# Optimization experiments

Measured on AMD Instinct MI355X. Metric: run time of the kernel, lower is better.

Reference implementation:

```python
import jax, jax.numpy as jnp
import numpy as np

B, N, D, H, L = 8, 1025, 1024, 8, 2   # N = maxlen + 1
NUM_BUCKETS = 64
EPS = 1e-8


def layernorm(x):
    mu = jnp.mean(x, axis=-1, keepdims=True)
    var = jnp.mean((x - mu) ** 2, axis=-1, keepdims=True)
    return (x - mu) / jnp.sqrt(var + EPS)


def rmsnorm(x):
    return x * jax.lax.rsqrt(jnp.mean(x * x, axis=-1, keepdims=True) + EPS)


def rel_attn_bias(action_ts, ts_w, pos_w):
    # positional part: pos_w[j - i + N - 1]  (equivalent to the pad/repeat trick)
    idx = jnp.arange(N)[None, :] - jnp.arange(N)[:, None] + (N - 1)  # [N,N] in [0,2N-2]
    rel_pos = pos_w[idx][None]  # [1,N,N]
    # time part: bucketize ext[i+1] - ext[j], ext = cat(ts, ts[:, N-1:N])
    ext = jnp.concatenate([action_ts, action_ts[:, N - 1:N]], axis=1)  # [B,N+1]
    diff = ext[:, 1:, None] - ext[:, None, :-1]  # [B,N,N]
    bucket = (jnp.log(jnp.clip(jnp.abs(diff), 1, None).astype(jnp.float32)) / 0.301).astype(jnp.int32)
    bucket = jnp.clip(bucket, 0, NUM_BUCKETS)
    rel_ts = ts_w[bucket]  # [B,N,N]
    return rel_pos + rel_ts


def hstu_block(x, mask, bias, qkvu, out_w, out_b, fc1_w, fc1_b, fc2_w, fc2_b):
    hd = D // H
    xn = layernorm(x)
    qkvu_act = jax.nn.silu(xn @ qkvu)  # [B,N,4D]
    q, k, v, u = jnp.split(qkvu_act, 4, axis=-1)
    q = q.reshape(B, N, H, hd)
    k = k.reshape(B, N, H, hd)
    v = v.reshape(B, N, H, hd)
    scores = jnp.einsum('bihd,bjhd->bhij', q, k) + bias[:, None]  # [B,H,N,N]
    attn = jax.nn.silu(scores) / N * mask[:, None]
    av = jnp.einsum('bhij,bjhd->bihd', attn, v).reshape(B, N, D)
    attn_out = (u * layernorm(av)) @ out_w + out_b
    h = x + attn_out
    # SwiGLU FFN (mult=2) with RMSNorm pre-norm and residual
    vg = rmsnorm(h) @ fc1_w + fc1_b  # [B,N,4D]
    vv, g = jnp.split(vg, 2, axis=-1)
    y = (jax.nn.silu(g) * vv) @ fc2_w + fc2_b
    return h + y


def setup_inputs() -> dict:
    key = jax.random.key(0)
    ks = jax.random.split(key, 12)
    std = 0.02
    seqs = jax.random.normal(ks[0], (B, N, D), jnp.float32)
    mask = jnp.tril(jnp.ones((N, N), jnp.float32))[None].repeat(B, axis=0)
    action_ts = jnp.sort(jax.random.randint(ks[1], (B, N), 0, 1000000000).astype(jnp.int64), axis=1)
    return {
        'seqs': seqs,
        'mask': mask,
        'action_ts': action_ts,
        'qkvu': jax.random.normal(ks[2], (L, D, 4 * D), jnp.float32) * std,
        'out_w': jax.random.normal(ks[3], (L, D, D), jnp.float32) * std,
        'out_b': jnp.zeros((L, D), jnp.float32),
        'ts_w': jax.random.normal(ks[4], (L, NUM_BUCKETS + 1), jnp.float32) * std,
        'pos_w': jax.random.normal(ks[5], (L, 2 * N - 1), jnp.float32) * std,
        'fc1_w': jax.random.normal(ks[6], (L, D, 4 * D), jnp.float32) * std,
        'fc1_b': jnp.zeros((L, 4 * D), jnp.float32),
        'fc2_w': jax.random.normal(ks[7], (L, 2 * D, D), jnp.float32) * std,
        'fc2_b': jnp.zeros((L, D), jnp.float32),
    }


def reference(seqs, mask, action_ts, qkvu, out_w, out_b, ts_w, pos_w, fc1_w, fc1_b, fc2_w, fc2_b):
    h = seqs
    for l in range(L):
        bias = rel_attn_bias(action_ts, ts_w[l], pos_w[l])
        h = hstu_block(h, mask, bias, qkvu[l], out_w[l], out_b[l],
                       fc1_w[l], fc1_b[l], fc2_w[l], fc2_b[l])
    return h
```

## Files before the change

### kernel.cpp

```cpp
#include <hip/hip_runtime.h>
#include <hip/hip_bf16.h>
#include <math.h>

#define BB 8
#define SEQN 1025
#define DD 1024
#define HH 8
#define HD 128
#define LL 2
#define MROWS (BB*SEQN)
#define NBUCKET 64

using short8 = __attribute__((ext_vector_type(8))) short;
using f32x4  = __attribute__((ext_vector_type(4))) float;
using f32x16 = __attribute__((ext_vector_type(16))) float;

__device__ __forceinline__ float silu_f(float x) { return x / (1.f + expf(-x)); }

__device__ __forceinline__ float bf2f(ushort u) {
  union { uint i; float f; } x; x.i = ((uint)u) << 16; return x.f;
}
__device__ __forceinline__ ushort f2bf(float f) {
  __hip_bfloat16 b = __float2bfloat16(f);
  return *reinterpret_cast<ushort*>(&b);
}
__device__ __forceinline__ void gll16(const void* g, void* l) {
  __builtin_amdgcn_global_load_lds((const __attribute__((address_space(1))) void*)g,
                                   (__attribute__((address_space(3))) void*)l, 16, 0, 0);
}
__device__ __forceinline__ uint pkbf(float lo, float hi) {
  uint r;
  asm("v_cvt_pk_bf16_f32 %0, %1, %2" : "=v"(r) : "v"(lo), "v"(hi));
  return r;
}
__device__ __forceinline__ f32x16 z16() {
  f32x16 v;
#pragma unroll
  for (int i = 0; i < 16; ++i) v[i] = 0.f;
  return v;
}

__global__ __launch_bounds__(256) void copy_kernel(const float* __restrict__ in,
                                                   float* __restrict__ out, int n4) {
  int idx = blockIdx.x * blockDim.x + threadIdx.x;
  int stride = gridDim.x * blockDim.x;
  const float4* i4 = (const float4*)in;
  float4* o4 = (float4*)out;
  for (int i = idx; i < n4; i += stride) o4[i] = i4[i];
}

__global__ __launch_bounds__(256) void wtrans(const float* __restrict__ W,
                                              ushort* __restrict__ Wt, int K, int N) {
  __shared__ float tile[32][33];
  int tid = threadIdx.x;
  int tx = tid & 31, ty = tid >> 5;
  int n0 = blockIdx.x * 32, k0 = blockIdx.y * 32;
#pragma unroll
  for (int r = 0; r < 32; r += 8)
    tile[ty + r][tx] = W[(size_t)(k0 + ty + r) * N + n0 + tx];
  __syncthreads();
#pragma unroll
  for (int r = 0; r < 32; r += 8)
    Wt[(size_t)(n0 + ty + r) * K + k0 + tx] = f2bf(tile[tx][ty + r]);
}

__global__ __launch_bounds__(256) void bias_kernel(const int* __restrict__ ts,
    const float* __restrict__ ts_w, const float* __restrict__ pos_w,
    float* __restrict__ biasT)
{
  int i = blockIdx.x * 256 + threadIdx.x;
  int j = blockIdx.y;
  int b = blockIdx.z;
  if (i >= SEQN) return;
  int ip1 = i + 1; if (ip1 > SEQN - 1) ip1 = SEQN - 1;
  long long t1 = (long long)ts[b * SEQN + ip1];
  long long t0 = (long long)ts[b * SEQN + j];
  long long d = t1 - t0;
  if (d < 0) d = -d;
  if (d < 1) d = 1;
  int bucket = (int)(logf((float)d) / 0.301f);
  if (bucket < 0) bucket = 0;
  if (bucket > NBUCKET) bucket = NBUCKET;
  biasT[((size_t)(b * SEQN + j)) * SEQN + i] = pos_w[j - i + SEQN - 1] + ts_w[bucket];
}

__global__ __launch_bounds__(256) void ln_kernel(const float* __restrict__ in,
                                                 ushort* __restrict__ out) {
  int row = blockIdx.x;
  int tid = threadIdx.x;
  const float* x = in + (size_t)row * DD;
  float4 v = *(const float4*)&x[tid * 4];
  float s = v.x + v.y + v.z + v.w;
  float ss = v.x*v.x + v.y*v.y + v.z*v.z + v.w*v.w;
#pragma unroll
  for (int off = 32; off >= 1; off >>= 1) { s += __shfl_xor(s, off); ss += __shfl_xor(ss, off); }
  __shared__ float red0[4], red1[4];
  if ((tid & 63) == 0) { red0[tid >> 6] = s; red1[tid >> 6] = ss; }
  __syncthreads();
  s = red0[0] + red0[1] + red0[2] + red0[3];
  ss = red1[0] + red1[1] + red1[2] + red1[3];
  float mu = s * (1.f / DD);
  float var = fmaxf(ss * (1.f / DD) - mu * mu, 0.f);
  float inv = 1.f / sqrtf(var + 1e-8f);
  ushort4 o;
  o.x = f2bf((v.x - mu) * inv); o.y = f2bf((v.y - mu) * inv);
  o.z = f2bf((v.z - mu) * inv); o.w = f2bf((v.w - mu) * inv);
  *(ushort4*)&out[(size_t)row * DD + tid * 4] = o;
}

__global__ __launch_bounds__(256) void rms_kernel(const float* __restrict__ in,
                                                  ushort* __restrict__ out) {
  int row = blockIdx.x;
  int tid = threadIdx.x;
  const float* x = in + (size_t)row * DD;
  float4 v = *(const float4*)&x[tid * 4];
  float ss = v.x*v.x + v.y*v.y + v.z*v.z + v.w*v.w;
#pragma unroll
  for (int off = 32; off >= 1; off >>= 1) ss += __shfl_xor(ss, off);
  __shared__ float red1[4];
  if ((tid & 63) == 0) red1[tid >> 6] = ss;
  __syncthreads();
  ss = red1[0] + red1[1] + red1[2] + red1[3];
  float inv = 1.f / sqrtf(ss * (1.f / DD) + 1e-8f);
  ushort4 o;
  o.x = f2bf(v.x * inv); o.y = f2bf(v.y * inv);
  o.z = f2bf(v.z * inv); o.w = f2bf(v.w * inv);
  *(ushort4*)&out[(size_t)row * DD + tid * 4] = o;
}

__global__ __launch_bounds__(256) void uln_kernel(const float* __restrict__ av,
    const ushort* __restrict__ act, ushort* __restrict__ out) {
  int row = blockIdx.x;
  int tid = threadIdx.x;
  const float* x = av + (size_t)row * DD;
  float4 v = *(const float4*)&x[tid * 4];
  float s = v.x + v.y + v.z + v.w;
  float ss = v.x*v.x + v.y*v.y + v.z*v.z + v.w*v.w;
#pragma unroll
  for (int off = 32; off >= 1; off >>= 1) { s += __shfl_xor(s, off); ss += __shfl_xor(ss, off); }
  __shared__ float red0[4], red1[4];
  if ((tid & 63) == 0) { red0[tid >> 6] = s; red1[tid >> 6] = ss; }
  __syncthreads();
  s = red0[0] + red0[1] + red0[2] + red0[3];
  ss = red1[0] + red1[1] + red1[2] + red1[3];
  float mu = s * (1.f / DD);
  float var = fmaxf(ss * (1.f / DD) - mu * mu, 0.f);
  float inv = 1.f / sqrtf(var + 1e-8f);
  ushort4 uu = *(const ushort4*)&act[(size_t)row * 4096 + 3072 + tid * 4];
  ushort4 o;
  o.x = f2bf(bf2f(uu.x) * (v.x - mu) * inv);
  o.y = f2bf(bf2f(uu.y) * (v.y - mu) * inv);
  o.z = f2bf(bf2f(uu.z) * (v.z - mu) * inv);
  o.w = f2bf(bf2f(uu.w) * (v.w - mu) * inv);
  *(ushort4*)&out[(size_t)row * DD + tid * 4] = o;
}

__global__ __launch_bounds__(256) void mgemm1(const ushort* __restrict__ A,
    const ushort* __restrict__ Bt, const float* __restrict__ bvec,
    float* __restrict__ Cout, int M, int Nn, int K)
{
  __shared__ ushort As[3][4096];
  __shared__ ushort Bs[3][4096];
  const int tid  = threadIdx.x;
  const int lane = tid & 63, wave = tid >> 6;
  const int wm = wave >> 1, wn = wave & 1;
  const int lrow = lane & 15, lk = lane >> 4;
  const int bm = blockIdx.y * 128, bn = blockIdx.x * 128;

  const ushort* Aga[2]; const ushort* Bga[2];
  ushort* Ada[2]; ushort* Bda[2];
#pragma unroll
  for (int i = 0; i < 2; ++i) {
    int c = tid + 256 * i;
    int row = c >> 2, s = c & 3;
    int sc = s ^ ((row >> 1) & 3);
    Aga[i] = A  + (size_t)(bm + row) * K + sc * 8;
    Bga[i] = Bt + (size_t)(bn + row) * K + sc * 8;
    Ada[i] = &As[0][c * 8];
    Bda[i] = &Bs[0][c * 8];
  }

  int aoff[4], boff[4];
#pragma unroll
  for (int m = 0; m < 4; ++m)
    aoff[m] = (wm * 64 + m * 16 + lrow) * 32 + ((lk ^ ((lrow >> 1) & 3)) * 8);
#pragma unroll
  for (int n = 0; n < 4; ++n)
    boff[n] = (wn * 64 + n * 16 + lrow) * 32 + ((lk ^ ((lrow >> 1) & 3)) * 8);

  f32x4 acc[4][4];
#pragma unroll
  for (int m = 0; m < 4; ++m)
#pragma unroll
    for (int n = 0; n < 4; ++n) acc[m][n] = (f32x4){0.f, 0.f, 0.f, 0.f};

  const int nk = K >> 5;
#pragma unroll
  for (int t = 0; t < 2; ++t) {
#pragma unroll
    for (int i = 0; i < 2; ++i) {
      gll16(Aga[i] + (t << 5), Ada[i] + t * 4096);
      gll16(Bga[i] + (t << 5), Bda[i] + t * 4096);
    }
  }
  int cur = 0, nxt2 = 2;
  for (int kt = 0; kt < nk; ++kt) {
    if (kt + 1 < nk) {
      asm volatile("s_waitcnt vmcnt(4)" ::: "memory");
    } else {
      asm volatile("s_waitcnt vmcnt(0)" ::: "memory");
    }
    __builtin_amdgcn_s_barrier();
    __builtin_amdgcn_sched_barrier(0);
    if (kt + 2 < nk) {
      const int ko = (kt + 2) << 5;
      const int bo = nxt2 * 4096;
#pragma unroll
      for (int i = 0; i < 2; ++i) {
        gll16(Aga[i] + ko, Ada[i] + bo);
        gll16(Bga[i] + ko, Bda[i] + bo);
      }
    }
    __builtin_amdgcn_s_setprio(1);
    {
      short8 af[4], bfr[4];
      const int co = cur * 4096;
#pragma unroll
      for (int m = 0; m < 4; ++m) af[m]  = *(const short8*)&As[0][co + aoff[m]];
#pragma unroll
      for (int n = 0; n < 4; ++n) bfr[n] = *(const short8*)&Bs[0][co + boff[n]];
#pragma unroll
      for (int m = 0; m < 4; ++m)
#pragma unroll
        for (int n = 0; n < 4; ++n)
          acc[m][n] = __builtin_amdgcn_mfma_f32_16x16x32_bf16(af[m], bfr[n], acc[m][n], 0, 0, 0);
    }
    __builtin_amdgcn_s_setprio(0);
    __builtin_amdgcn_sched_barrier(0);
    cur = (cur == 2) ? 0 : cur + 1;
    nxt2 = (nxt2 == 2) ? 0 : nxt2 + 1;
  }

  const int colbase = bn + wn * 64 + lrow;
  const int rowbase = bm + wm * 64 + lk * 4;
#pragma unroll
  for (int m = 0; m < 4; ++m) {
    int row0 = rowbase + m * 16;
#pragma unroll
    for (int n = 0; n < 4; ++n) {
      int col = colbase + n * 16;
      float bv = bvec[col];
#pragma unroll
      for (int r = 0; r < 4; ++r) {
        int row = row0 + r;
        if (row < M) {
          float* p = Cout + (size_t)row * Nn + col;
          *p += acc[m][n][r] + bv;
        }
      }
    }
  }
}

template<int MODE, int BM, int BN>
__global__ __launch_bounds__(512, 2) void mgemm2(const ushort* __restrict__ A,
    const ushort* __restrict__ Bt, const float* __restrict__ bvec,
    void* __restrict__ Cout, int M, int Nn, int K)
{
  constexpr int ACH = BM / 64;
  constexpr int BCH = BN / 64;
  constexpr int MF  = BM / 32;
  constexpr int NF  = BN / 64;
  constexpr int AUS = BM * 64;
  constexpr int LDSU = (BM + BN) * 64;
  __shared__ ushort LS[2][LDSU];

  const int tid = threadIdx.x;
  const int lane = tid & 63, wave = tid >> 6;
  const int wm = wave >> 2, wn = wave & 3;
  const int lrow = lane & 15, lk = lane >> 4;
  const int bm = blockIdx.y * BM, bn = blockIdx.x * BN;

  const ushort* Ag[ACH]; const ushort* Bg[BCH];
  int Ald[ACH], Bld[BCH];
#pragma unroll
  for (int i = 0; i < ACH; ++i) {
    int c = tid + 512 * i, row = c >> 3, s = c & 7;
    Ag[i] = A + (size_t)(bm + row) * K + (s ^ (row & 7)) * 8;
    Ald[i] = c * 8;
  }
#pragma unroll
  for (int i = 0; i < BCH; ++i) {
    int c = tid + 512 * i, row = c >> 3, s = c & 7;
    int gr;
    if (MODE == 3) {
      gr = blockIdx.x * 128 + (row >> 5) * 16 + ((row >> 4) & 1) * 2048 + (row & 15);
    } else {
      gr = bn + row;
    }
    Bg[i] = Bt + (size_t)gr * K + (s ^ (row & 7)) * 8;
    Bld[i] = AUS + c * 8;
  }
  int aoff[MF], boff[NF];
#pragma unroll
  for (int m = 0; m < MF; ++m) {
    int row = wm * (BM / 2) + m * 16 + lrow;
    aoff[m] = row * 64 + ((lk ^ (lrow & 7)) * 8);
  }
#pragma unroll
  for (int n = 0; n < NF; ++n) {
    int row = wn * (BN / 4) + n * 16 + lrow;
    boff[n] = AUS + row * 64 + ((lk ^ (lrow & 7)) * 8);
  }

  f32x4 acc[MF][NF];
#pragma unroll
  for (int m = 0; m < MF; ++m)
#pragma unroll
    for (int n = 0; n < NF; ++n) acc[m][n] = (f32x4){0.f, 0.f, 0.f, 0.f};

  const int NT = K >> 6;

#define STAGE_TILE(T, B)                                        \
  {                                                             \
    const int _ko = (T) << 6;                                   \
    _Pragma("unroll")                                           \
    for (int i = 0; i < ACH; ++i) gll16(Ag[i] + _ko, &LS[B][Ald[i]]); \
    _Pragma("unroll")                                           \
    for (int i = 0; i < BCH; ++i) gll16(Bg[i] + _ko, &LS[B][Bld[i]]); \
  }

  STAGE_TILE(0, 0);
  __syncthreads();
  for (int t = 0; t < NT; ++t) {
    const int buf = t & 1;
    if (t + 1 < NT) STAGE_TILE(t + 1, buf ^ 1);
    short8 bfr[NF][2];
#pragma unroll
    for (int n = 0; n < NF; ++n) {
      bfr[n][0] = *(const short8*)&LS[buf][boff[n]];
      bfr[n][1] = *(const short8*)&LS[buf][boff[n] ^ 32];
    }
#pragma unroll
    for (int m = 0; m < MF; ++m) {
      short8 af0 = *(const short8*)&LS[buf][aoff[m]];
      short8 af1 = *(const short8*)&LS[buf][aoff[m] ^ 32];
      __builtin_amdgcn_s_setprio(1);
#pragma unroll
      for (int n = 0; n < NF; ++n) {
        acc[m][n] = __builtin_amdgcn_mfma_f32_16x16x32_bf16(af0, bfr[n][0], acc[m][n], 0, 0, 0);
        acc[m][n] = __builtin_amdgcn_mfma_f32_16x16x32_bf16(af1, bfr[n][1], acc[m][n], 0, 0, 0);
      }
      __builtin_amdgcn_s_setprio(0);
    }
    __syncthreads();
  }
#undef STAGE_TILE

  const int rowb0 = bm + wm * (BM / 2) + lk * 4;
  if (MODE == 0) {
    const int colb0 = bn + wn * (BN / 4) + lrow;
    __hip_bfloat16* Cb = (__hip_bfloat16*)Cout;
#pragma unroll
    for (int m = 0; m < MF; ++m) {
      int row0 = rowb0 + m * 16;
#pragma unroll
      for (int n = 0; n < NF; ++n) {
        int col = colb0 + n * 16;
#pragma unroll
        for (int r = 0; r < 4; ++r) {
          int row = row0 + r;
          if (row < M)
            Cb[(size_t)row * Nn + col] = __float2bfloat16(silu_f(acc[m][n][r]));
        }
      }
    }
  } else {
    __hip_bfloat16* Cb = (__hip_bfloat16*)Cout;
#pragma unroll
    for (int q = 0; q < 2; ++q) {
      int vcol = blockIdx.x * 128 + (2 * wn + q) * 16 + lrow;
      float bvv = bvec[vcol];
      float bvg = bvec[vcol + 2048];
#pragma unroll
      for (int m = 0; m < MF; ++m) {
        int row0 = rowb0 + m * 16;
#pragma unroll
        for (int r = 0; r < 4; ++r) {
          int row = row0 + r;
          if (row < M) {
            float v = acc[m][2 * q][r] + bvv;
            float g = acc[m][2 * q + 1][r] + bvg;
            Cb[(size_t)row * 2048 + vcol] = __float2bfloat16(silu_f(g) * v);
          }
        }
      }
    }
  }
}

__global__ __launch_bounds__(256) void attn_kernel(const ushort* __restrict__ act,
    const float* __restrict__ biasT, float* __restrict__ av)
{
  __shared__ __align__(16) char KL[8192];
  __shared__ __align__(16) char VL[8320];
  const int tid = threadIdx.x;
  const int l = tid & 63, w = tid >> 6;
  const int qi = (int)(gridDim.x - 1 - blockIdx.x);
  const int i0 = qi * 128;
  const int h = blockIdx.y, b = blockIdx.z;
  const int lo31 = l & 31, hi = l >> 5;

  const int jlim = (i0 + 128 < SEQN) ? i0 + 128 : SEQN;
  const int nt = (jlim + 31) >> 5;

  const int gi_q = i0 + w * 32 + lo31;
  const int gi_qc = gi_q < SEQN ? gi_q : SEQN - 1;
  const size_t actB = (size_t)b * SEQN;
  const ushort* qrow = act + (actB + gi_qc) * 4096 + h * HD;
  short8 qreg[8];
#pragma unroll
  for (int dc = 0; dc < 8; ++dc)
    qreg[dc] = *(const short8*)(qrow + dc * 16 + hi * 8);

  f32x16 acc[4];
#pragma unroll
  for (int dt = 0; dt < 4; ++dt) acc[dt] = z16();

  const int id0 = tid, id1 = tid + 256;
  const int j_0 = id0 >> 4, c8_0 = (id0 & 15) * 8;
  const int j_1 = id1 >> 4, c8_1 = (id1 & 15) * 8;
  char* kw0 = KL + j_0 * 256 + (((id0 & 15) ^ (j_0 & 15)) << 4);
  char* kw1 = KL + j_1 * 256 + (((id1 & 15) ^ (j_1 & 15)) << 4);
  char* vw0 = VL + ((id0 & 15) >> 1) * 1040 + j_0 * 32 + (id0 & 1) * 16;
  char* vw1 = VL + ((id1 & 15) >> 1) * 1040 + j_1 * 32 + (id1 & 1) * 16;
  const uint vbase = (uint)(size_t)(__attribute__((address_space(3))) char*)
      (VL + ((l >> 4) & 1) * 1040 + hi * 256 + (l & 15) * 8);

  short8 kr0, kr1, vr0, vr1;
  {
    const ushort* p0 = act + (actB + j_0) * 4096 + 1024 + h * HD + c8_0;
    const ushort* p1 = act + (actB + j_1) * 4096 + 1024 + h * HD + c8_1;
    kr0 = *(const short8*)p0; vr0 = *(const short8*)(p0 + 1024);
    kr1 = *(const short8*)p1; vr1 = *(const short8*)(p1 + 1024);
  }
  const float invN = 1.f / (float)SEQN;
  const int gi0w = i0 + w * 32;

  for (int t = 0; t < nt; ++t) {
    const int j0 = t * 32;
    __syncthreads();
    *(short8*)kw0 = kr0; *(short8*)kw1 = kr1;
    *(short8*)vw0 = vr0; *(short8*)vw1 = vr1;
    __syncthreads();
    if (t + 1 < nt) {
      const ushort* p0 = act + (actB + j0 + 32 + j_0) * 4096 + 1024 + h * HD + c8_0;
      const ushort* p1 = act + (actB + j0 + 32 + j_1) * 4096 + 1024 + h * HD + c8_1;
      kr0 = *(const short8*)p0; vr0 = *(const short8*)(p0 + 1024);
      kr1 = *(const short8*)p1; vr1 = *(const short8*)(p1 + 1024);
    }
    if (j0 <= gi0w + 31 && gi0w < SEQN) {
      float bv[16];
#pragma unroll
      for (int r = 0; r < 16; ++r) {
        int j = (r & 3) + 8 * (r >> 2) + 4 * hi;
        int gj = j0 + j;
        int gjc = gj < SEQN ? gj : SEQN - 1;
        bv[r] = biasT[(actB + gjc) * SEQN + gi_qc];
      }
      f32x16 st = z16();
#pragma unroll
      for (int dc = 0; dc < 8; ++dc) {
        short8 kf = *(const short8*)(KL + lo31 * 256 + ((((dc << 1) + hi) ^ (lo31 & 15)) << 4));
        st = __builtin_amdgcn_mfma_f32_32x32x16_bf16(kf, qreg[dc], st, 0, 0, 0);
      }
      float p[16];
#pragma unroll
      for (int r = 0; r < 16; ++r) {
        int j = (r & 3) + 8 * (r >> 2) + 4 * hi;
        int gj = j0 + j;
        float s = st[r] + bv[r];
        float pw = s * __builtin_amdgcn_rcpf(1.f + __expf(-s)) * invN;
        p[r] = ((gj <= gi_q) && (gi_q < SEQN)) ? pw : 0.f;
      }
      short8 paf[2];
#pragma unroll
      for (int g = 0; g < 2; ++g) {
        uint w0 = pkbf(p[g * 8 + 0], p[g * 8 + 1]);
        uint w2 = pkbf(p[g * 8 + 4], p[g * 8 + 5]);
        uint w1 = pkbf(p[g * 8 + 2], p[g * 8 + 3]);
        uint w3 = pkbf(p[g * 8 + 6], p[g * 8 + 7]);
        asm volatile("v_permlane32_swap_b32 %0, %1" : "+v"(w0), "+v"(w2));
        asm volatile("v_permlane32_swap_b32 %0, %1" : "+v"(w1), "+v"(w3));
        union UF { uint u[4]; short8 s; } uf;
        uf.u[0] = w0; uf.u[1] = w1; uf.u[2] = w2; uf.u[3] = w3;
        paf[g] = uf.s;
      }
      uint64_t v00, v01, v02, v03, v10, v11, v12, v13, v20, v21, v22, v23, v30, v31, v32, v33;
      asm volatile(
        "ds_read_b64_tr_b16 %0, %16 offset:0\n\t"
        "ds_read_b64_tr_b16 %1, %16 offset:128\n\t"
        "ds_read_b64_tr_b16 %2, %16 offset:512\n\t"
        "ds_read_b64_tr_b16 %3, %16 offset:640\n\t"
        "ds_read_b64_tr_b16 %4, %16 offset:2080\n\t"
        "ds_read_b64_tr_b16 %5, %16 offset:2208\n\t"
        "ds_read_b64_tr_b16 %6, %16 offset:2592\n\t"
        "ds_read_b64_tr_b16 %7, %16 offset:2720\n\t"
        "ds_read_b64_tr_b16 %8, %16 offset:4160\n\t"
        "ds_read_b64_tr_b16 %9, %16 offset:4288\n\t"
        "ds_read_b64_tr_b16 %10, %16 offset:4672\n\t"
        "ds_read_b64_tr_b16 %11, %16 offset:4800\n\t"
        "ds_read_b64_tr_b16 %12, %16 offset:6240\n\t"
        "ds_read_b64_tr_b16 %13, %16 offset:6368\n\t"
        "ds_read_b64_tr_b16 %14, %16 offset:6752\n\t"
        "ds_read_b64_tr_b16 %15, %16 offset:6880\n\t"
        "s_waitcnt lgkmcnt(0)"
        : "=v"(v00), "=v"(v01), "=v"(v02), "=v"(v03),
          "=v"(v10), "=v"(v11), "=v"(v12), "=v"(v13),
          "=v"(v20), "=v"(v21), "=v"(v22), "=v"(v23),
          "=v"(v30), "=v"(v31), "=v"(v32), "=v"(v33)
        : "v"(vbase) : "memory");
      union UV { uint64_t q[2]; short8 s; };
      { UV uv; uv.q[0] = v00; uv.q[1] = v01;
        acc[0] = __builtin_amdgcn_mfma_f32_32x32x16_bf16(paf[0], uv.s, acc[0], 0, 0, 0); }
      { UV uv; uv.q[0] = v02; uv.q[1] = v03;
        acc[0] = __builtin_amdgcn_mfma_f32_32x32x16_bf16(paf[1], uv.s, acc[0], 0, 0, 0); }
      { UV uv; uv.q[0] = v10; uv.q[1] = v11;
        acc[1] = __builtin_amdgcn_mfma_f32_32x32x16_bf16(paf[0], uv.s, acc[1], 0, 0, 0); }
      { UV uv; uv.q[0] = v12; uv.q[1] = v13;
        acc[1] = __builtin_amdgcn_mfma_f32_32x32x16_bf16(paf[1], uv.s, acc[1], 0, 0, 0); }
      { UV uv; uv.q[0] = v20; uv.q[1] = v21;
        acc[2] = __builtin_amdgcn_mfma_f32_32x32x16_bf16(paf[0], uv.s, acc[2], 0, 0, 0); }
      { UV uv; uv.q[0] = v22; uv.q[1] = v23;
        acc[2] = __builtin_amdgcn_mfma_f32_32x32x16_bf16(paf[1], uv.s, acc[2], 0, 0, 0); }
      { UV uv; uv.q[0] = v30; uv.q[1] = v31;
        acc[3] = __builtin_amdgcn_mfma_f32_32x32x16_bf16(paf[0], uv.s, acc[3], 0, 0, 0); }
      { UV uv; uv.q[0] = v32; uv.q[1] = v33;
        acc[3] = __builtin_amdgcn_mfma_f32_32x32x16_bf16(paf[1], uv.s, acc[3], 0, 0, 0); }
    }
  }
#pragma unroll
  for (int dt = 0; dt < 4; ++dt) {
#pragma unroll
    for (int r = 0; r < 16; ++r) {
      int q = (r & 3) + 8 * (r >> 2) + 4 * hi;
      int gi = i0 + w * 32 + q;
      if (gi < SEQN)
        av[(actB + gi) * DD + h * HD + dt * 32 + lo31] = acc[dt][r];
    }
  }
}

extern "C" void kernel_launch(void* const* d_in, const int* in_sizes, int n_in,
                              void* d_out, int out_size, void* d_ws, size_t ws_size,
                              hipStream_t stream) {
  const float* seqs  = (const float*)d_in[0];
  const int*   ts    = (const int*)d_in[2];
  const float* qkvuW = (const float*)d_in[3];
  const float* outW  = (const float*)d_in[4];
  const float* outB  = (const float*)d_in[5];
  const float* tsW   = (const float*)d_in[6];
  const float* posW  = (const float*)d_in[7];
  const float* fc1W  = (const float*)d_in[8];
  const float* fc1B  = (const float*)d_in[9];
  const float* fc2W  = (const float*)d_in[10];
  const float* fc2B  = (const float*)d_in[11];
  float* h = (float*)d_out;
  char* ws = (char*)d_ws;

  ushort* xn    = (ushort*)(ws);
  ushort* act   = (ushort*)(ws + 17301504);
  ushort* gated = (ushort*)(ws + 84475904);
  float*  biasT = (float*) (ws + 118554624);
  float*  av    = (float*) (ws + 152174624);
  ushort* wq    = (ushort*)(ws + 185761824);
  ushort* wo    = (ushort*)(ws + 194150432);
  ushort* wf1   = (ushort*)(ws + 196247584);
  ushort* wf2   = (ushort*)(ws + 204636192);

  copy_kernel<<<2048, 256, 0, stream>>>(seqs, h, MROWS * DD / 4);

  for (int l = 0; l < LL; l++) {
    wtrans<<<dim3(128, 32), 256, 0, stream>>>(qkvuW + (size_t)l * DD * 4096, wq, DD, 4096);
    wtrans<<<dim3(32, 32),  256, 0, stream>>>(outW  + (size_t)l * DD * DD,   wo, DD, DD);
    wtrans<<<dim3(128, 32), 256, 0, stream>>>(fc1W  + (size_t)l * DD * 4096, wf1, DD, 4096);
    wtrans<<<dim3(32, 64),  256, 0, stream>>>(fc2W  + (size_t)l * 2048 * DD, wf2, 2048, DD);

    bias_kernel<<<dim3(5, SEQN, BB), 256, 0, stream>>>(
        ts, tsW + l * (NBUCKET + 1), posW + l * (2 * SEQN - 1), biasT);

    ln_kernel<<<MROWS, 256, 0, stream>>>(h, xn);
    mgemm2<0, 256, 256><<<dim3(16, 33), 512, 0, stream>>>(xn, wq, nullptr, act, MROWS, 4096, DD);
    attn_kernel<<<dim3(9, HH, BB), 256, 0, stream>>>(act, biasT, av);
    uln_kernel<<<MROWS, 256, 0, stream>>>(av, act, xn);
    mgemm1<<<dim3(8, 65), 256, 0, stream>>>(xn, wo, outB + l * DD, h, MROWS, DD, DD);
    rms_kernel<<<MROWS, 256, 0, stream>>>(h, xn);
    mgemm2<3, 256, 256><<<dim3(16, 33), 512, 0, stream>>>(xn, wf1, fc1B + (size_t)l * 4096, gated, MROWS, 2048, DD);
    mgemm1<<<dim3(8, 65), 256, 0, stream>>>(gated, wf2, fc2B + l * DD, h, MROWS, DD, 2048);
  }
}
```

Measured before the change: 1.083 ms.

## Replace 512-thread GEMM with 256x128 tile, K=32 pipelined kernel using explicit waitcnt

Replaces the mgemm2 kernel used for the QKVU and FC1 GEMMs with a new mgemm3 kernel. The new kernel uses 4 waves on a 256x128 output tile and a K step of 32. It switches to separate A/B LDS buffers with a 4-chunk swizzle. Prefetch of the next tile is overlapped using an explicit s_waitcnt vmcnt plus raw s_barrier with sched_barrier fences, replacing __syncthreads. The aim is better occupancy and finer-grained load/compute overlap, at the cost of less reuse per K step and more barriers per iteration.

Result: slower. 1.492 ms (+37.7%).

```diff
diff --git a/kernel.cpp b/kernel.cpp
--- a/kernel.cpp
+++ b/kernel.cpp
@@ -262,110 +262,103 @@
   }
 }
 
-template<int MODE, int BM, int BN>
-__global__ __launch_bounds__(512, 2) void mgemm2(const ushort* __restrict__ A,
+template<int MODE>
+__global__ __launch_bounds__(256) void mgemm3(const ushort* __restrict__ A,
     const ushort* __restrict__ Bt, const float* __restrict__ bvec,
     void* __restrict__ Cout, int M, int Nn, int K)
 {
-  constexpr int ACH = BM / 64;
-  constexpr int BCH = BN / 64;
-  constexpr int MF  = BM / 32;
-  constexpr int NF  = BN / 64;
-  constexpr int AUS = BM * 64;
-  constexpr int LDSU = (BM + BN) * 64;
-  __shared__ ushort LS[2][LDSU];
-
+  __shared__ ushort As[2][8192];
+  __shared__ ushort Bs[2][4096];
   const int tid = threadIdx.x;
   const int lane = tid & 63, wave = tid >> 6;
-  const int wm = wave >> 2, wn = wave & 3;
+  const int wm = wave >> 1, wn = wave & 1;
   const int lrow = lane & 15, lk = lane >> 4;
-  const int bm = blockIdx.y * BM, bn = blockIdx.x * BN;
-
-  const ushort* Ag[ACH]; const ushort* Bg[BCH];
-  int Ald[ACH], Bld[BCH];
-#pragma unroll
-  for (int i = 0; i < ACH; ++i) {
-    int c = tid + 512 * i, row = c >> 3, s = c & 7;
-    Ag[i] = A + (size_t)(bm + row) * K + (s ^ (row & 7)) * 8;
+  const int bm = blockIdx.y * 256;
+
+  const ushort* Ag[4]; const ushort* Bg[2];
+  int Ald[4], Bld[2];
+#pragma unroll
+  for (int i = 0; i < 4; ++i) {
+    int c = tid + 256 * i, row = c >> 2, s = c & 3;
+    Ag[i] = A + (size_t)(bm + row) * K + (s ^ ((row >> 1) & 3)) * 8;
     Ald[i] = c * 8;
   }
 #pragma unroll
-  for (int i = 0; i < BCH; ++i) {
-    int c = tid + 512 * i, row = c >> 3, s = c & 7;
+  for (int i = 0; i < 2; ++i) {
+    int c = tid + 256 * i, row = c >> 2, s = c & 3;
     int gr;
     if (MODE == 3) {
-      gr = blockIdx.x * 128 + (row >> 5) * 16 + ((row >> 4) & 1) * 2048 + (row & 15);
+      gr = blockIdx.x * 64 + (row >> 5) * 16 + ((row >> 4) & 1) * 2048 + (row & 15);
     } else {
-      gr = bn + row;
-    }
-    Bg[i] = Bt + (size_t)gr * K + (s ^ (row & 7)) * 8;
-    Bld[i] = AUS + c * 8;
-  }
-  int aoff[MF], boff[NF];
-#pragma unroll
-  for (int m = 0; m < MF; ++m) {
-    int row = wm * (BM / 2) + m * 16 + lrow;
-    aoff[m] = row * 64 + ((lk ^ (lrow & 7)) * 8);
-  }
-#pragma unroll
-  for (int n = 0; n < NF; ++n) {
-    int row = wn * (BN / 4) + n * 16 + lrow;
-    boff[n] = AUS + row * 64 + ((lk ^ (lrow & 7)) * 8);
-  }
-
-  f32x4 acc[MF][NF];
-#pragma unroll
-  for (int m = 0; m < MF; ++m)
-#pragma unroll
-    for (int n = 0; n < NF; ++n) acc[m][n] = (f32x4){0.f, 0.f, 0.f, 0.f};
-
-  const int NT = K >> 6;
-
-#define STAGE_TILE(T, B)                                        \
-  {                                                             \
-    const int _ko = (T) << 6;                                   \
-    _Pragma("unroll")                                           \
-    for (int i = 0; i < ACH; ++i) gll16(Ag[i] + _ko, &LS[B][Ald[i]]); \
-    _Pragma("unroll")                                           \
-    for (int i = 0; i < BCH; ++i) gll16(Bg[i] + _ko, &LS[B][Bld[i]]); \
-  }
-
-  STAGE_TILE(0, 0);
-  __syncthreads();
+      gr = blockIdx.x * 128 + row;
+    }
+    Bg[i] = Bt + (size_t)gr * K + (s ^ ((row >> 1) & 3)) * 8;
+    Bld[i] = c * 8;
+  }
+  int aoff[8], boff[4];
+#pragma unroll
+  for (int m = 0; m < 8; ++m)
+    aoff[m] = (wm * 128 + m * 16 + lrow) * 32 + ((lk ^ ((lrow >> 1) & 3)) * 8);
+#pragma unroll
+  for (int n = 0; n < 4; ++n)
+    boff[n] = (wn * 64 + n * 16 + lrow) * 32 + ((lk ^ ((lrow >> 1) & 3)) * 8);
+
+  f32x4 acc[8][4];
+#pragma unroll
+  for (int m = 0; m < 8; ++m)
+#pragma unroll
+    for (int n = 0; n < 4; ++n) acc[m][n] = (f32x4){0.f, 0.f, 0.f, 0.f};
+
+  const int NT = K >> 5;
+
+#define STAGE3(T, B)                                                  \
+  {                                                                   \
+    const int _ko = (T) << 5;                                         \
+    _Pragma("unroll")                                                 \
+    for (int i = 0; i < 4; ++i) gll16(Ag[i] + _ko, &As[B][Ald[i]]);   \
+    _Pragma("unroll")                                                 \
+    for (int i = 0; i < 2; ++i) gll16(Bg[i] + _ko, &Bs[B][Bld[i]]);   \
+  }
+
+  STAGE3(0, 0);
   for (int t = 0; t < NT; ++t) {
     const int buf = t & 1;
-    if (t + 1 < NT) STAGE_TILE(t + 1, buf ^ 1);
-    short8 bfr[NF][2];
-#pragma unroll
-    for (int n = 0; n < NF; ++n) {
-      bfr[n][0] = *(const short8*)&LS[buf][boff[n]];
-      bfr[n][1] = *(const short8*)&LS[buf][boff[n] ^ 32];
-    }
-#pragma unroll
-    for (int m = 0; m < MF; ++m) {
-      short8 af0 = *(const short8*)&LS[buf][aoff[m]];
-      short8 af1 = *(const short8*)&LS[buf][aoff[m] ^ 32];
-      __builtin_amdgcn_s_setprio(1);
-#pragma unroll
-      for (int n = 0; n < NF; ++n) {
-        acc[m][n] = __builtin_amdgcn_mfma_f32_16x16x32_bf16(af0, bfr[n][0], acc[m][n], 0, 0, 0);
-        acc[m][n] = __builtin_amdgcn_mfma_f32_16x16x32_bf16(af1, bfr[n][1], acc[m][n], 0, 0, 0);
-      }
-      __builtin_amdgcn_s_setprio(0);
-    }
-    __syncthreads();
-  }
-#undef STAGE_TILE
-
-  const int rowb0 = bm + wm * (BM / 2) + lk * 4;
+    if (t + 1 < NT) {
+      STAGE3(t + 1, buf ^ 1);
+      asm volatile("s_waitcnt vmcnt(6)" ::: "memory");
+    } else {
+      asm volatile("s_waitcnt vmcnt(0)" ::: "memory");
+    }
+    __builtin_amdgcn_s_barrier();
+    __builtin_amdgcn_sched_barrier(0);
+    __builtin_amdgcn_s_setprio(1);
+    {
+      short8 bfr[4];
+#pragma unroll
+      for (int n = 0; n < 4; ++n) bfr[n] = *(const short8*)&Bs[buf][boff[n]];
+#pragma unroll
+      for (int m = 0; m < 8; ++m) {
+        short8 af = *(const short8*)&As[buf][aoff[m]];
+#pragma unroll
+        for (int n = 0; n < 4; ++n)
+          acc[m][n] = __builtin_amdgcn_mfma_f32_16x16x32_bf16(af, bfr[n], acc[m][n], 0, 0, 0);
+      }
+    }
+    __builtin_amdgcn_s_setprio(0);
+    __builtin_amdgcn_sched_barrier(0);
+    __builtin_amdgcn_s_barrier();
+  }
+#undef STAGE3
+
+  const int rowb0 = bm + wm * 128 + lk * 4;
   if (MODE == 0) {
-    const int colb0 = bn + wn * (BN / 4) + lrow;
+    const int colb0 = blockIdx.x * 128 + wn * 64 + lrow;
     __hip_bfloat16* Cb = (__hip_bfloat16*)Cout;
 #pragma unroll
-    for (int m = 0; m < MF; ++m) {
+    for (int m = 0; m < 8; ++m) {
       int row0 = rowb0 + m * 16;
 #pragma unroll
-      for (int n = 0; n < NF; ++n) {
+      for (int n = 0; n < 4; ++n) {
         int col = colb0 + n * 16;
 #pragma unroll
         for (int r = 0; r < 4; ++r) {
@@ -379,11 +372,11 @@
     __hip_bfloat16* Cb = (__hip_bfloat16*)Cout;
 #pragma unroll
     for (int q = 0; q < 2; ++q) {
-      int vcol = blockIdx.x * 128 + (2 * wn + q) * 16 + lrow;
+      int vcol = blockIdx.x * 64 + (2 * wn + q) * 16 + lrow;
       float bvv = bvec[vcol];
       float bvg = bvec[vcol + 2048];
 #pragma unroll
-      for (int m = 0; m < MF; ++m) {
+      for (int m = 0; m < 8; ++m) {
         int row0 = rowb0 + m * 16;
 #pragma unroll
         for (int r = 0; r < 4; ++r) {
@@ -590,12 +583,12 @@
         ts, tsW + l * (NBUCKET + 1), posW + l * (2 * SEQN - 1), biasT);
 
     ln_kernel<<<MROWS, 256, 0, stream>>>(h, xn);
-    mgemm2<0, 256, 256><<<dim3(16, 33), 512, 0, stream>>>(xn, wq, nullptr, act, MROWS, 4096, DD);
+    mgemm3<0><<<dim3(32, 33), 256, 0, stream>>>(xn, wq, nullptr, act, MROWS, 4096, DD);
     attn_kernel<<<dim3(9, HH, BB), 256, 0, stream>>>(act, biasT, av);
     uln_kernel<<<MROWS, 256, 0, stream>>>(av, act, xn);
     mgemm1<<<dim3(8, 65), 256, 0, stream>>>(xn, wo, outB + l * DD, h, MROWS, DD, DD);
     rms_kernel<<<MROWS, 256, 0, stream>>>(h, xn);
-    mgemm2<3, 256, 256><<<dim3(16, 33), 512, 0, stream>>>(xn, wf1, fc1B + (size_t)l * 4096, gated, MROWS, 2048, DD);
+    mgemm3<3><<<dim3(32, 33), 256, 0, stream>>>(xn, wf1, fc1B + (size_t)l * 4096, gated, MROWS, 2048, DD);
     mgemm1<<<dim3(8, 65), 256, 0, stream>>>(gated, wf2, fc2B + l * DD, h, MROWS, DD, 2048);
   }
 }
```
